# Kernel tuning notes

Measured on AMD Instinct MI355X. Metric: run time of the kernel, lower is better.

The kernel has to match this reference:

```python
import jax, jax.numpy as jnp
import numpy as np

N = 8_000_000   # total nodes across the batch
B = 2048        # number of graphs (segments)
L1 = 1.0 / 50.0


def _bce(p, t):
    # elementwise BCE matching torch.nn.BCELoss: logs clamped at -100
    logp = jnp.clip(jnp.log(p), -100.0)
    log1mp = jnp.clip(jnp.log1p(-p), -100.0)
    return -(t * logp + (1.0 - t) * log1mp)


def setup_inputs() -> dict:
    key = jax.random.key(0)
    k1, k2, k3, k4, k5, k6 = jax.random.split(key, 6)
    y_mus_pred = jax.random.uniform(k1, (N,), dtype=jnp.float32)
    y_mus = jax.random.uniform(k2, (N,), dtype=jnp.float32)
    y_sat_pred = jax.random.uniform(k3, (B,), dtype=jnp.float32)
    y_sat = jax.random.uniform(k4, (B,), dtype=jnp.float32)
    batch = jnp.sort(jax.random.randint(k5, (N,), 0, B, dtype=jnp.int32))
    mask = jax.random.randint(k6, (N,), 0, 2, dtype=jnp.int32)
    return {"y_mus_pred": y_mus_pred, "y_mus": y_mus,
            "y_sat_pred": y_sat_pred, "y_sat": y_sat,
            "batch": batch, "mask": mask}


def reference(y_mus_pred, y_mus, y_sat_pred, y_sat, batch, mask):
    m = mask.astype(y_mus_pred.dtype)
    # per-node BCE on masked predictions (torch: bce_mus(pred*mask, target), reduction='sum' per graph)
    bce = _bce(y_mus_pred * m, y_mus)                      # [N]
    seg_bce = jax.ops.segment_sum(bce, batch, num_segments=B)  # [B]
    seg_cnt = jax.ops.segment_sum(m, batch, num_segments=B)    # [B] = sum(mask) per graph
    per_graph = jnp.where(seg_cnt > 0, seg_bce / jnp.maximum(seg_cnt, 1.0), 0.0)
    total = per_graph.sum()
    # scalar saturation BCE (mean reduction) scaled by L1
    total = total + _bce(y_sat_pred, y_sat).mean() * jnp.asarray(L1, y_sat_pred.dtype)
    return total
```

## Files before the change

### kernel.cpp

```cpp
#include <hip/hip_runtime.h>

#define BLOCK  256
#define NB     2048
#define CHUNK  1024
#define FBLK   1024
#define MAXSEG 2048

typedef float fx4 __attribute__((ext_vector_type(4)));
typedef int   ix4 __attribute__((ext_vector_type(4)));

__device__ __forceinline__ float bce_elem(float p, float t) {
    float lp  = fmaxf(__logf(p), -100.0f);
    float l1p = fmaxf(__logf(1.0f - p), -100.0f);
    return -__builtin_fmaf(t, lp - l1p, l1p);
}

__global__ __launch_bounds__(BLOCK, 8) void stream_kernel(
    const float* __restrict__ pred, const float* __restrict__ tgt,
    const int* __restrict__ batch, const int* __restrict__ mask,
    int* __restrict__ eseg, float* __restrict__ eb, float* __restrict__ ec,
    float* __restrict__ gbins_b, float* __restrict__ gbins_c,
    int n, int nchunks)
{
    const int tid = threadIdx.x;
    const int wid = tid >> 6;

    __shared__ float red[BLOCK / 64][4];

    for (int c = blockIdx.x; c < nchunks; c += NB) {
        const int base = c << 10;
        const int i4   = (base >> 2) + tid;
        const int e0   = base + (tid << 2);
        const int s0   = batch[base];
        const int last = min(base + CHUNK - 1, n - 1);
        const int sL   = batch[last];

        float a0b = 0.f, a0c = 0.f, a1b = 0.f, a1c = 0.f;

        if (e0 + 3 < n) {
            fx4 p = *(reinterpret_cast<const fx4*>(pred)  + i4);
            fx4 t = *(reinterpret_cast<const fx4*>(tgt)   + i4);
            ix4 m = *(reinterpret_cast<const ix4*>(mask)  + i4);
            ix4 s = *(reinterpret_cast<const ix4*>(batch) + i4);
            #pragma unroll
            for (int j = 0; j < 4; ++j) {
                float mf = (float)m[j];
                float v  = bce_elem(p[j] * mf, t[j]);
                int   se = s[j];
                if (se == s0)      { a0b += v; a0c += mf; }
                else if (se == sL) { a1b += v; a1c += mf; }
                else {
                    atomicAdd(&gbins_b[se], v);
                    atomicAdd(&gbins_c[se], mf);
                }
            }
        } else if (e0 < n) {
            for (int j = 0; j < 4 && e0 + j < n; ++j) {
                const int e  = e0 + j;
                float mf = (float)mask[e];
                float v  = bce_elem(pred[e] * mf, tgt[e]);
                int   se = batch[e];
                if (se == s0)      { a0b += v; a0c += mf; }
                else if (se == sL) { a1b += v; a1c += mf; }
                else { atomicAdd(&gbins_b[se], v); atomicAdd(&gbins_c[se], mf); }
            }
        }

        #pragma unroll
        for (int o = 32; o > 0; o >>= 1) {
            a0b += __shfl_xor(a0b, o);  a0c += __shfl_xor(a0c, o);
            a1b += __shfl_xor(a1b, o);  a1c += __shfl_xor(a1c, o);
        }
        if ((tid & 63) == 0) {
            red[wid][0] = a0b;  red[wid][1] = a0c;
            red[wid][2] = a1b;  red[wid][3] = a1c;
        }
        __syncthreads();
        if (tid == 0) {
            float sb0 = 0, sc0 = 0, sb1 = 0, sc1 = 0;
            #pragma unroll
            for (int w = 0; w < BLOCK / 64; ++w) {
                sb0 += red[w][0];  sc0 += red[w][1];
                sb1 += red[w][2];  sc1 += red[w][3];
            }
            eseg[2 * c]     = s0;  eb[2 * c]     = sb0;  ec[2 * c]     = sc0;
            eseg[2 * c + 1] = sL;  eb[2 * c + 1] = sb1;  ec[2 * c + 1] = sc1;
        }
        __syncthreads();
    }
}

__global__ __launch_bounds__(FBLK) void finalize_kernel(
    const int* __restrict__ eseg, const float* __restrict__ eb,
    const float* __restrict__ ec,
    const float* __restrict__ gbins_b, const float* __restrict__ gbins_c,
    const float* __restrict__ sat_pred, const float* __restrict__ sat_tgt,
    float* __restrict__ out, int nentries, int Bseg)
{
    __shared__ float bb[MAXSEG];
    __shared__ float bc[MAXSEG];
    const int tid = threadIdx.x;
    for (int i = tid; i < Bseg; i += FBLK) { bb[i] = 0.f; bc[i] = 0.f; }
    __syncthreads();

    const int per = (nentries + FBLK - 1) / FBLK;
    const int lo  = tid * per;
    const int hi  = min(lo + per, nentries);
    if (lo < hi) {
        int   cur = eseg[lo];
        float ab = 0.f, ac = 0.f;
        for (int i = lo; i < hi; ++i) {
            const int s = eseg[i];
            if (s != cur) {
                atomicAdd(&bb[cur], ab);  atomicAdd(&bc[cur], ac);
                cur = s;  ab = 0.f;  ac = 0.f;
            }
            ab += eb[i];  ac += ec[i];
        }
        atomicAdd(&bb[cur], ab);  atomicAdd(&bc[cur], ac);
    }
    __syncthreads();

    float local = 0.f;
    for (int i = tid; i < Bseg; i += FBLK) {
        const float cnt  = bc[i] + gbins_c[i];
        const float bsum = bb[i] + gbins_b[i];
        float pg = (cnt > 0.f) ? bsum / fmaxf(cnt, 1.f) : 0.f;
        pg += bce_elem(sat_pred[i], sat_tgt[i]) * ((1.0f / 50.0f) / (float)Bseg);
        local += pg;
    }
    #pragma unroll
    for (int o = 32; o > 0; o >>= 1) local += __shfl_xor(local, o);
    __shared__ float ws[FBLK / 64];
    if ((tid & 63) == 0) ws[tid >> 6] = local;
    __syncthreads();
    if (tid == 0) {
        float s = 0.f;
        #pragma unroll
        for (int w = 0; w < FBLK / 64; ++w) s += ws[w];
        out[0] = s;
    }
}

extern "C" void kernel_launch(void* const* d_in, const int* in_sizes, int n_in,
                              void* d_out, int out_size, void* d_ws, size_t ws_size,
                              hipStream_t stream) {
    const float* y_mus_pred = (const float*)d_in[0];
    const float* y_mus      = (const float*)d_in[1];
    const float* y_sat_pred = (const float*)d_in[2];
    const float* y_sat      = (const float*)d_in[3];
    const int*   batch      = (const int*)d_in[4];
    const int*   mask       = (const int*)d_in[5];

    const int n    = in_sizes[0];
    const int Bseg = in_sizes[2];

    const int nchunks  = (n + CHUNK - 1) / CHUNK;
    const int nentries = 2 * nchunks;

    int*   eseg = (int*)d_ws;
    float* eb   = (float*)(eseg + nentries);
    float* ec   = eb + nentries;
    float* gb   = ec + nentries;
    float* gc   = gb + Bseg;

    hipMemsetAsync(gb, 0, 2 * Bseg * sizeof(float), stream);
    stream_kernel<<<NB, BLOCK, 0, stream>>>(
        y_mus_pred, y_mus, batch, mask, eseg, eb, ec, gb, gc, n, nchunks);
    finalize_kernel<<<1, FBLK, 0, stream>>>(
        eseg, eb, ec, gb, gc, y_sat_pred, y_sat, (float*)d_out, nentries, Bseg);
}
```

Before: 182.2 us.

## Replace batch array streaming with binary-searched segment boundaries and parallel finalize

Adds a kernel that binary-searches the sorted batch array for each segment's start offset, so the main streaming pass no longer reads the batch array. That removes about a quarter of its memory traffic and uses nontemporal loads for the rest. Chunks spanning more than two segments fall back to per-element table lookups and atomics. The single-block finalize is replaced by a per-graph kernel that atomically adds partial sums into the output. The cost is an extra launch, an extra memset, and nondeterministic float summation order.

```diff
diff --git a/kernel.cpp b/kernel.cpp
--- a/kernel.cpp
+++ b/kernel.cpp
@@ -1,10 +1,8 @@
 #include <hip/hip_runtime.h>
 
-#define BLOCK  256
-#define NB     2048
-#define CHUNK  1024
-#define FBLK   1024
-#define MAXSEG 2048
+#define BLOCK 256
+#define NB    2048
+#define CHUNK 1024
 
 typedef float fx4 __attribute__((ext_vector_type(4)));
 typedef int   ix4 __attribute__((ext_vector_type(4)));
@@ -15,54 +13,110 @@
     return -__builtin_fmaf(t, lp - l1p, l1p);
 }
 
+__device__ __forceinline__ int wave_lower_bound(const int* __restrict__ a, int n, int v) {
+    const int lane = threadIdx.x & 63;
+    int lo = 0, hi = n;
+    while (hi - lo > 64) {
+        int range  = hi - lo;
+        int stride = range / 65 + 1;
+        int idx    = lo + (lane + 1) * stride;
+        bool lt    = (idx < hi) && (a[idx] < v);
+        int  c     = __popcll(__ballot(lt));
+        int  nlo   = lo + c * stride;
+        int  nhi   = nlo + stride;
+        if (nhi > hi) nhi = hi;
+        lo = nlo; hi = nhi;
+    }
+    int idx = lo + lane;
+    bool ge = (idx >= hi) || (a[idx] >= v);
+    unsigned long long bal = __ballot(ge);
+    return bal ? (lo + __ffsll(bal) - 1) : hi;
+}
+
+__global__ __launch_bounds__(256) void bounds_kernel(
+    const int* __restrict__ batch, int* __restrict__ st, int n, int Bseg)
+{
+    const int W = blockIdx.x * 4 + (threadIdx.x >> 6);
+    if (W <= Bseg) {
+        int r = wave_lower_bound(batch, n, W);
+        if ((threadIdx.x & 63) == 0) st[W] = r;
+    }
+}
+
+__device__ __forceinline__ int seg_of_tab(const int* __restrict__ st,
+                                          int Bseg, int n, int e) {
+    int s = (int)(((long long)e * (long long)Bseg) / (long long)n);
+    if (s > Bseg - 1) s = Bseg - 1;
+    while (st[s] > e) --s;
+    while (st[s + 1] <= e) ++s;
+    return s;
+}
+
 __global__ __launch_bounds__(BLOCK, 8) void stream_kernel(
     const float* __restrict__ pred, const float* __restrict__ tgt,
-    const int* __restrict__ batch, const int* __restrict__ mask,
+    const int* __restrict__ mask, const int* __restrict__ st,
     int* __restrict__ eseg, float* __restrict__ eb, float* __restrict__ ec,
-    float* __restrict__ gbins_b, float* __restrict__ gbins_c,
-    int n, int nchunks)
+    float* __restrict__ gb, float* __restrict__ gc,
+    int n, int Bseg, int nchunks)
 {
     const int tid = threadIdx.x;
     const int wid = tid >> 6;
 
+    __shared__ int   sh_s0, sh_sL, sh_bnd, sh_simple;
     __shared__ float red[BLOCK / 64][4];
 
     for (int c = blockIdx.x; c < nchunks; c += NB) {
         const int base = c << 10;
-        const int i4   = (base >> 2) + tid;
-        const int e0   = base + (tid << 2);
-        const int s0   = batch[base];
         const int last = min(base + CHUNK - 1, n - 1);
-        const int sL   = batch[last];
+
+        if (tid == 0) {
+            const int s0 = seg_of_tab(st, Bseg, n, base);
+            const int sL = seg_of_tab(st, Bseg, n, last);
+            sh_s0  = s0;
+            sh_sL  = sL;
+            sh_bnd = st[sL];
+            sh_simple = (st[s0 + 1] >= st[sL]) ? 1 : 0;
+        }
+        __syncthreads();
+        const int s0 = sh_s0, sL = sh_sL, bnd = sh_bnd, simple = sh_simple;
 
         float a0b = 0.f, a0c = 0.f, a1b = 0.f, a1c = 0.f;
-
-        if (e0 + 3 < n) {
-            fx4 p = *(reinterpret_cast<const fx4*>(pred)  + i4);
-            fx4 t = *(reinterpret_cast<const fx4*>(tgt)   + i4);
-            ix4 m = *(reinterpret_cast<const ix4*>(mask)  + i4);
-            ix4 s = *(reinterpret_cast<const ix4*>(batch) + i4);
-            #pragma unroll
+        const int e0 = base + (tid << 2);
+
+        if (simple) {
+            if (e0 + 3 < n) {
+                fx4 p = __builtin_nontemporal_load(
+                            reinterpret_cast<const fx4*>(pred) + (e0 >> 2));
+                fx4 t = __builtin_nontemporal_load(
+                            reinterpret_cast<const fx4*>(tgt)  + (e0 >> 2));
+                ix4 m = __builtin_nontemporal_load(
+                            reinterpret_cast<const ix4*>(mask) + (e0 >> 2));
+                #pragma unroll
+                for (int j = 0; j < 4; ++j) {
+                    float mf = (float)m[j];
+                    float v  = bce_elem(p[j] * mf, t[j]);
+                    if (e0 + j < bnd) { a0b += v; a0c += mf; }
+                    else              { a1b += v; a1c += mf; }
+                }
+            } else if (e0 < n) {
+                for (int j = 0; j < 4 && e0 + j < n; ++j) {
+                    const int e  = e0 + j;
+                    float mf = (float)mask[e];
+                    float v  = bce_elem(pred[e] * mf, tgt[e]);
+                    if (e < bnd) { a0b += v; a0c += mf; }
+                    else         { a1b += v; a1c += mf; }
+                }
+            }
+        } else {
             for (int j = 0; j < 4; ++j) {
-                float mf = (float)m[j];
-                float v  = bce_elem(p[j] * mf, t[j]);
-                int   se = s[j];
-                if (se == s0)      { a0b += v; a0c += mf; }
-                else if (se == sL) { a1b += v; a1c += mf; }
-                else {
-                    atomicAdd(&gbins_b[se], v);
-                    atomicAdd(&gbins_c[se], mf);
+                const int e = e0 + j;
+                if (e < n) {
+                    float mf = (float)mask[e];
+                    float v  = bce_elem(pred[e] * mf, tgt[e]);
+                    const int s = seg_of_tab(st, Bseg, n, e);
+                    atomicAdd(&gb[s], v);
+                    atomicAdd(&gc[s], mf);
                 }
-            }
-        } else if (e0 < n) {
-            for (int j = 0; j < 4 && e0 + j < n; ++j) {
-                const int e  = e0 + j;
-                float mf = (float)mask[e];
-                float v  = bce_elem(pred[e] * mf, tgt[e]);
-                int   se = batch[e];
-                if (se == s0)      { a0b += v; a0c += mf; }
-                else if (se == sL) { a1b += v; a1c += mf; }
-                else { atomicAdd(&gbins_b[se], v); atomicAdd(&gbins_c[se], mf); }
             }
         }
 
@@ -90,56 +144,43 @@
     }
 }
 
-__global__ __launch_bounds__(FBLK) void finalize_kernel(
-    const int* __restrict__ eseg, const float* __restrict__ eb,
-    const float* __restrict__ ec,
-    const float* __restrict__ gbins_b, const float* __restrict__ gbins_c,
+__global__ __launch_bounds__(256) void pergraph_kernel(
+    const int* __restrict__ st, const int* __restrict__ eseg,
+    const float* __restrict__ eb, const float* __restrict__ ec,
+    const float* __restrict__ gb, const float* __restrict__ gc,
     const float* __restrict__ sat_pred, const float* __restrict__ sat_tgt,
-    float* __restrict__ out, int nentries, int Bseg)
+    float* __restrict__ out, int Bseg)
 {
-    __shared__ float bb[MAXSEG];
-    __shared__ float bc[MAXSEG];
-    const int tid = threadIdx.x;
-    for (int i = tid; i < Bseg; i += FBLK) { bb[i] = 0.f; bc[i] = 0.f; }
+    const int tid  = threadIdx.x;
+    const int wid  = tid >> 6;
+    const int lane = tid & 63;
+    const int S    = blockIdx.x * 4 + wid;
+
+    float pg = 0.f;
+    if (S < Bseg) {
+        float sb = 0.f, sc = 0.f;
+        const int ss = st[S], se = st[S + 1];
+        if (ss < se) {
+            const int ilo = 2 * (ss >> 10);
+            const int ihi = 2 * ((se - 1) >> 10) + 1;
+            for (int i = ilo + lane; i <= ihi; i += 64) {
+                if (eseg[i] == S) { sb += eb[i]; sc += ec[i]; }
+            }
+        }
+        if (lane == 0) { sb += gb[S]; sc += gc[S]; }
+        #pragma unroll
+        for (int o = 32; o > 0; o >>= 1) {
+            sb += __shfl_xor(sb, o);  sc += __shfl_xor(sc, o);
+        }
+        if (lane == 0) {
+            pg = (sc > 0.f) ? sb / fmaxf(sc, 1.f) : 0.f;
+            pg += bce_elem(sat_pred[S], sat_tgt[S]) * ((1.0f / 50.0f) / (float)Bseg);
+        }
+    }
+    __shared__ float ws[4];
+    if (lane == 0) ws[wid] = pg;
     __syncthreads();
-
-    const int per = (nentries + FBLK - 1) / FBLK;
-    const int lo  = tid * per;
-    const int hi  = min(lo + per, nentries);
-    if (lo < hi) {
-        int   cur = eseg[lo];
-        float ab = 0.f, ac = 0.f;
-        for (int i = lo; i < hi; ++i) {
-            const int s = eseg[i];
-            if (s != cur) {
-                atomicAdd(&bb[cur], ab);  atomicAdd(&bc[cur], ac);
-                cur = s;  ab = 0.f;  ac = 0.f;
-            }
-            ab += eb[i];  ac += ec[i];
-        }
-        atomicAdd(&bb[cur], ab);  atomicAdd(&bc[cur], ac);
-    }
-    __syncthreads();
-
-    float local = 0.f;
-    for (int i = tid; i < Bseg; i += FBLK) {
-        const float cnt  = bc[i] + gbins_c[i];
-        const float bsum = bb[i] + gbins_b[i];
-        float pg = (cnt > 0.f) ? bsum / fmaxf(cnt, 1.f) : 0.f;
-        pg += bce_elem(sat_pred[i], sat_tgt[i]) * ((1.0f / 50.0f) / (float)Bseg);
-        local += pg;
-    }
-    #pragma unroll
-    for (int o = 32; o > 0; o >>= 1) local += __shfl_xor(local, o);
-    __shared__ float ws[FBLK / 64];
-    if ((tid & 63) == 0) ws[tid >> 6] = local;
-    __syncthreads();
-    if (tid == 0) {
-        float s = 0.f;
-        #pragma unroll
-        for (int w = 0; w < FBLK / 64; ++w) s += ws[w];
-        out[0] = s;
-    }
+    if (tid == 0) atomicAdd(out, (ws[0] + ws[1]) + (ws[2] + ws[3]));
 }
 
 extern "C" void kernel_launch(void* const* d_in, const int* in_sizes, int n_in,
@@ -155,18 +196,21 @@
     const int n    = in_sizes[0];
     const int Bseg = in_sizes[2];
 
-    const int nchunks  = (n + CHUNK - 1) / CHUNK;
-    const int nentries = 2 * nchunks;
-
-    int*   eseg = (int*)d_ws;
-    float* eb   = (float*)(eseg + nentries);
-    float* ec   = eb + nentries;
-    float* gb   = ec + nentries;
+    const int nchunks = (n + CHUNK - 1) / CHUNK;
+
+    int*   st   = (int*)d_ws;
+    int*   eseg = st + (Bseg + 1);
+    float* eb   = (float*)(eseg + 2 * nchunks);
+    float* ec   = eb + 2 * nchunks;
+    float* gb   = ec + 2 * nchunks;
     float* gc   = gb + Bseg;
 
     hipMemsetAsync(gb, 0, 2 * Bseg * sizeof(float), stream);
+    hipMemsetAsync(d_out, 0, sizeof(float), stream);
+
+    bounds_kernel<<<(Bseg + 4) / 4, 256, 0, stream>>>(batch, st, n, Bseg);
     stream_kernel<<<NB, BLOCK, 0, stream>>>(
-        y_mus_pred, y_mus, batch, mask, eseg, eb, ec, gb, gc, n, nchunks);
-    finalize_kernel<<<1, FBLK, 0, stream>>>(
-        eseg, eb, ec, gb, gc, y_sat_pred, y_sat, (float*)d_out, nentries, Bseg);
-}
+        y_mus_pred, y_mus, mask, st, eseg, eb, ec, gb, gc, n, Bseg, nchunks);
+    pergraph_kernel<<<(Bseg + 3) / 4, 256, 0, stream>>>(
+        st, eseg, eb, ec, gb, gc, y_sat_pred, y_sat, (float*)d_out, Bseg);
+}
```

Measured after the change: 162.7 us. 1.12x faster.
